# Performance work log

Measured on AMD Instinct MI355X. Metric: run time of the kernel, lower is better.

Reference implementation:

```python
import jax, jax.numpy as jnp
import numpy as np

B, S, D, H, DFF, L, R, V = 2, 1024, 1024, 16, 4096, 2, 3, 32000
HD = D // H


def layer_norm(x, g, b, eps=1e-5):
    mu = jnp.mean(x, axis=-1, keepdims=True)
    var = jnp.var(x, axis=-1, keepdims=True)
    return (x - mu) / jnp.sqrt(var + eps) * g + b


def recursion_block(x, mask, Wqkv, bqkv, Wo, bo, W1, b1, W2, b2, ln1_g, ln1_b, ln2_g, ln2_b):
    # shared pre-LN transformer stack of L layers, applied once per recursion step
    Bc, Sc, _ = x.shape
    scale = 1.0 / np.sqrt(HD).astype(np.float32)
    for l in range(L):
        h = layer_norm(x, ln1_g[l], ln1_b[l])
        qkv = h @ Wqkv[l] + bqkv[l]
        q, k, v = jnp.split(qkv, 3, axis=-1)
        q = q.reshape(Bc, Sc, H, HD).transpose(0, 2, 1, 3)
        k = k.reshape(Bc, Sc, H, HD).transpose(0, 2, 1, 3)
        v = v.reshape(Bc, Sc, H, HD).transpose(0, 2, 1, 3)
        scores = jnp.einsum('bhqd,bhkd->bhqk', q, k) * scale + mask
        attn = jax.nn.softmax(scores, axis=-1)
        o = jnp.einsum('bhqk,bhkd->bhqd', attn, v).transpose(0, 2, 1, 3).reshape(Bc, Sc, D)
        x = x + o @ Wo[l] + bo[l]
        h2 = layer_norm(x, ln2_g[l], ln2_b[l])
        x = x + jax.nn.gelu(h2 @ W1[l] + b1[l]) @ W2[l] + b2[l]
    return x


def setup_inputs() -> dict:
    key = jax.random.key(0)
    ks = jax.random.split(key, 12)
    n = lambda k, shape: (jax.random.normal(k, shape, jnp.float32) * 0.02)
    return {
        'input_ids': jax.random.randint(ks[0], (B, S), 0, V),
        'token_embed': n(ks[1], (V, D)),
        'pos_embed': n(ks[2], (S, D)),
        'Wqkv': n(ks[3], (L, D, 3 * D)), 'bqkv': jnp.zeros((L, 3 * D), jnp.float32),
        'Wo': n(ks[4], (L, D, D)), 'bo': jnp.zeros((L, D), jnp.float32),
        'W1': n(ks[5], (L, D, DFF)), 'b1': jnp.zeros((L, DFF), jnp.float32),
        'W2': n(ks[6], (L, DFF, D)), 'b2': jnp.zeros((L, D), jnp.float32),
        'ln1_g': jnp.ones((L, D), jnp.float32), 'ln1_b': jnp.zeros((L, D), jnp.float32),
        'ln2_g': jnp.ones((L, D), jnp.float32), 'ln2_b': jnp.zeros((L, D), jnp.float32),
        'final_g': jnp.ones((D,), jnp.float32), 'final_b': jnp.zeros((D,), jnp.float32),
        'Wr': n(ks[7], (D, R)), 'br': jnp.zeros((R,), jnp.float32),
    }


def reference(input_ids, token_embed, pos_embed, Wqkv, bqkv, Wo, bo, W1, b1, W2, b2,
              ln1_g, ln1_b, ln2_g, ln2_b, final_g, final_b, Wr, br):
    h = token_embed[input_ids] + pos_embed[None, :, :]            # [B,S,D]
    mask = jnp.where(jnp.tril(jnp.ones((S, S), bool)), 0.0, -jnp.inf)[None, None]  # [1,1,S,S]
    # token-choice router on detached hidden states
    rlogits = jax.lax.stop_gradient(h) @ Wr + br                  # [B,S,R]
    probs = jax.nn.softmax(rlogits, axis=-1)
    depth_map = jnp.argmax(rlogits, axis=-1) + 1                  # depths in 1..R
    importance = probs.mean(axis=(0, 1))
    router_loss = R * jnp.sum(importance ** 2)                    # load-balance aux loss
    res = h
    for step in range(R):
        step_mask = depth_map >= step + 1                         # [B,S] bool
        upd = recursion_block(res, mask, Wqkv, bqkv, Wo, bo, W1, b1, W2, b2,
                              ln1_g, ln1_b, ln2_g, ln2_b)
        res = jnp.where(step_mask[..., None], upd, res)
    hf = layer_norm(res, final_g, final_b)
    logits = hf @ token_embed.T                                   # tied lm_head
    return logits, depth_map, router_loss
```

## Files before the change

kernel.cpp:

```cpp
#include <hip/hip_runtime.h>
#include <hip/hip_bf16.h>

#define DD 1024
#define SS 1024
#define BB 2
#define HH 16
#define DFFN 4096
#define LLAYERS 2
#define RSTEPS 3
#define VV 32000
#define NTOK (BB*SS)

typedef __attribute__((ext_vector_type(8))) short s16x8;
typedef __attribute__((ext_vector_type(8))) __bf16 bf16x8;
typedef __attribute__((ext_vector_type(4))) float f32x4;

__device__ __forceinline__ unsigned short f2bf(float f) {
  unsigned int u = __float_as_uint(f);
  u += 0x7FFFu + ((u >> 16) & 1u);
  return (unsigned short)(u >> 16);
}

__device__ __forceinline__ f32x4 mfma16(s16x8 a, s16x8 b, f32x4 c) {
  return __builtin_amdgcn_mfma_f32_16x16x32_bf16(
      __builtin_bit_cast(bf16x8, a), __builtin_bit_cast(bf16x8, b), c, 0, 0, 0);
}

__device__ __forceinline__ void gload16(const unsigned short* g, unsigned short* l) {
  __builtin_amdgcn_global_load_lds(
      (const __attribute__((address_space(1))) unsigned int*)(const void*)g,
      (__attribute__((address_space(3))) unsigned int*)(void*)l, 16, 0, 0);
}

#define BAR()  asm volatile("s_barrier" ::: "memory")
#define LGK0() do { asm volatile("s_waitcnt lgkmcnt(0)" ::: "memory"); \
                    __builtin_amdgcn_sched_barrier(0); } while (0)
#define VM4()  asm volatile("s_waitcnt vmcnt(4)" ::: "memory")
#define VM0()  asm volatile("s_waitcnt vmcnt(0)" ::: "memory")

__global__ __launch_bounds__(256) void wtrans_all_kernel(
    const float* __restrict__ Wqkv, const float* __restrict__ Wo,
    const float* __restrict__ W1, const float* __restrict__ W2,
    const float* __restrict__ te,
    unsigned short* __restrict__ WqkvT, unsigned short* __restrict__ WoT,
    unsigned short* __restrict__ W1T, unsigned short* __restrict__ W2T,
    unsigned short* __restrict__ teb) {
  const int bid = blockIdx.x;
  const int tid = threadIdx.x;
  if (bid >= 6144) {
    long i = ((long)(bid - 6144) * 256 + tid) * 8;
    float4 v0 = *(const float4*)(te + i);
    float4 v1 = *(const float4*)(te + i + 4);
    ushort4 a, b;
    a.x = f2bf(v0.x); a.y = f2bf(v0.y); a.z = f2bf(v0.z); a.w = f2bf(v0.w);
    b.x = f2bf(v1.x); b.y = f2bf(v1.y); b.z = f2bf(v1.z); b.w = f2bf(v1.w);
    *(ushort4*)(teb + i) = a;
    *(ushort4*)(teb + i + 4) = b;
    return;
  }
  const float* src; unsigned short* dst; int Kd, Nd, local;
  if (bid < 1536) {
    int l = (bid >= 768);
    local = bid - l * 768;
    src = Wqkv + (long)l * DD * 3 * DD; dst = WqkvT + (long)l * 3 * DD * DD;
    Kd = DD; Nd = 3 * DD;
  } else if (bid < 2048) {
    int l = (bid - 1536) >> 8; local = (bid - 1536) & 255;
    src = Wo + (long)l * DD * DD; dst = WoT + (long)l * DD * DD;
    Kd = DD; Nd = DD;
  } else if (bid < 4096) {
    int l = (bid - 2048) >> 10; local = (bid - 2048) & 1023;
    src = W1 + (long)l * DD * DFFN; dst = W1T + (long)l * DFFN * DD;
    Kd = DD; Nd = DFFN;
  } else {
    int l = (bid - 4096) >> 10; local = (bid - 4096) & 1023;
    src = W2 + (long)l * DFFN * DD; dst = W2T + (long)l * DD * DFFN;
    Kd = DFFN; Nd = DD;
  }
  const int tn = Nd >> 6;
  const int n0 = (local % tn) * 64, k0 = (local / tn) * 64;
  __shared__ unsigned short t[64][68];
#pragma unroll
  for (int c = 0; c < 4; ++c) {
    int p = tid + c * 256;
    int kr = p >> 4, nc = (p & 15) * 4;
    float4 v = *(const float4*)(src + (long)(k0 + kr) * Nd + n0 + nc);
    t[nc + 0][kr] = f2bf(v.x);
    t[nc + 1][kr] = f2bf(v.y);
    t[nc + 2][kr] = f2bf(v.z);
    t[nc + 3][kr] = f2bf(v.w);
  }
  __syncthreads();
#pragma unroll
  for (int c = 0; c < 4; ++c) {
    int p = tid + c * 256;
    int nr = p >> 4, kc = (p & 15) * 4;
    ushort4 o;
    o.x = t[nr][kc]; o.y = t[nr][kc + 1]; o.z = t[nr][kc + 2]; o.w = t[nr][kc + 3];
    *(ushort4*)(dst + (long)(n0 + nr) * Kd + k0 + kc) = o;
  }
}

__global__ __launch_bounds__(256) void embed_router_kernel(
    const int* __restrict__ ids, const float* __restrict__ te,
    const float* __restrict__ pe, const float* __restrict__ Wr,
    const float* __restrict__ br, float* __restrict__ res,
    float* __restrict__ probs, float* __restrict__ depth_ws,
    float* __restrict__ out_depth) {
  int row = blockIdx.x;
  int s = row & (SS - 1);
  int id = ids[row];
  int t = threadIdx.x;
  int d = t * 4;
  float4 a = *(const float4*)(te + (long)id * DD + d);
  float4 p = *(const float4*)(pe + (long)s * DD + d);
  float4 o; o.x = a.x + p.x; o.y = a.y + p.y; o.z = a.z + p.z; o.w = a.w + p.w;
  *(float4*)(res + (long)row * DD + d) = o;
  float a0 = 0.f, a1 = 0.f, a2 = 0.f;
  float hv[4] = {o.x, o.y, o.z, o.w};
#pragma unroll
  for (int j = 0; j < 4; ++j) {
    int dd = d + j;
    a0 += hv[j] * Wr[dd * 3 + 0];
    a1 += hv[j] * Wr[dd * 3 + 1];
    a2 += hv[j] * Wr[dd * 3 + 2];
  }
  for (int off = 32; off; off >>= 1) {
    a0 += __shfl_down(a0, off);
    a1 += __shfl_down(a1, off);
    a2 += __shfl_down(a2, off);
  }
  __shared__ float red[4][3];
  int wave = t >> 6;
  if ((t & 63) == 0) { red[wave][0] = a0; red[wave][1] = a1; red[wave][2] = a2; }
  __syncthreads();
  if (t == 0) {
    a0 = red[0][0] + red[1][0] + red[2][0] + red[3][0] + br[0];
    a1 = red[0][1] + red[1][1] + red[2][1] + red[3][1] + br[1];
    a2 = red[0][2] + red[1][2] + red[2][2] + red[3][2] + br[2];
    float m = fmaxf(a0, fmaxf(a1, a2));
    float e0 = expf(a0 - m), e1 = expf(a1 - m), e2 = expf(a2 - m);
    float inv = 1.f / (e0 + e1 + e2);
    probs[row * 3 + 0] = e0 * inv;
    probs[row * 3 + 1] = e1 * inv;
    probs[row * 3 + 2] = e2 * inv;
    int am = 0; float bv = a0;
    if (a1 > bv) { bv = a1; am = 1; }
    if (a2 > bv) { bv = a2; am = 2; }
    float dm = (float)(am + 1);
    depth_ws[row] = dm;
    out_depth[row] = dm;
  }
}

__global__ __launch_bounds__(256) void router_finalize_kernel(
    const float* __restrict__ probs, float* __restrict__ out_loss) {
  __shared__ float red[256][3];
  int t = threadIdx.x;
  float s0 = 0.f, s1 = 0.f, s2 = 0.f;
  for (int r = t; r < NTOK; r += 256) {
    s0 += probs[r * 3 + 0]; s1 += probs[r * 3 + 1]; s2 += probs[r * 3 + 2];
  }
  red[t][0] = s0; red[t][1] = s1; red[t][2] = s2;
  __syncthreads();
  for (int off = 128; off; off >>= 1) {
    if (t < off) {
      red[t][0] += red[t + off][0];
      red[t][1] += red[t + off][1];
      red[t][2] += red[t + off][2];
    }
    __syncthreads();
  }
  if (t == 0) {
    float i0 = red[0][0] / NTOK, i1 = red[0][1] / NTOK, i2 = red[0][2] / NTOK;
    out_loss[0] = (float)RSTEPS * (i0 * i0 + i1 * i1 + i2 * i2);
  }
}

__global__ __launch_bounds__(256) void ln_kernel(
    const float* __restrict__ x, const float* __restrict__ g,
    const float* __restrict__ b, unsigned short* __restrict__ y) {
  int row = blockIdx.x;
  int t = threadIdx.x;
  float4 v = *(const float4*)(x + (long)row * DD + t * 4);
  float s = v.x + v.y + v.z + v.w;
  float q = v.x * v.x + v.y * v.y + v.z * v.z + v.w * v.w;
  for (int off = 32; off; off >>= 1) {
    s += __shfl_down(s, off);
    q += __shfl_down(q, off);
  }
  __shared__ float rs[4], rq[4];
  int wave = t >> 6;
  if ((t & 63) == 0) { rs[wave] = s; rq[wave] = q; }
  __syncthreads();
  float S_ = rs[0] + rs[1] + rs[2] + rs[3];
  float Q_ = rq[0] + rq[1] + rq[2] + rq[3];
  float mu = S_ * (1.f / DD);
  float var = Q_ * (1.f / DD) - mu * mu;
  float rstd = rsqrtf(var + 1e-5f);
  int d = t * 4;
  float4 gg = *(const float4*)(g + d);
  float4 bb = *(const float4*)(b + d);
  ushort4 ov;
  ov.x = f2bf((v.x - mu) * rstd * gg.x + bb.x);
  ov.y = f2bf((v.y - mu) * rstd * gg.y + bb.y);
  ov.z = f2bf((v.z - mu) * rstd * gg.z + bb.z);
  ov.w = f2bf((v.w - mu) * rstd * gg.w + bb.w);
  *(ushort4*)(y + (long)row * DD + d) = ov;
}

__device__ __forceinline__ void stageA8(unsigned short* S, int buf, int qm,
    const unsigned short* A, int lda, long m0, int kt, int tid) {
  unsigned short* dst = S + buf * 32768 + qm * 8192;
#pragma unroll
  for (int c = 0; c < 2; ++c) {
    int idx = tid + c * 512;
    int L = (idx << 4) ^ (((idx >> 5) & 1) << 5);
    int band = L >> 13, row = (L >> 7) & 63, kel = (L & 127) >> 1;
    gload16(A + (m0 + band * 128 + qm * 64 + row) * (long)lda + kt * 64 + kel,
            dst + idx * 8);
  }
}

__device__ __forceinline__ void stageB8(unsigned short* S, int buf, int qn,
    const unsigned short* Bt, int ldb, long n0, int kt, int tid) {
  unsigned short* dst = S + buf * 32768 + 16384 + qn * 8192;
#pragma unroll
  for (int c = 0; c < 2; ++c) {
    int idx = tid + c * 512;
    int L = (idx << 4) ^ (((idx >> 5) & 1) << 5);
    int band = L >> 12, row = (L >> 7) & 31, kel = (L & 127) >> 1;
    gload16(Bt + (n0 + band * 64 + qn * 32 + row) * (long)ldb + kt * 64 + kel,
            dst + idx * 8);
  }
}

__device__ __forceinline__ void read_af8(const unsigned short* S, int base,
    int wm, int l16, int g, s16x8 af[2][4]) {
  const int swz = ((l16 >> 2) & 1) << 5;
#pragma unroll
  for (int kk = 0; kk < 2; ++kk)
#pragma unroll
    for (int mf = 0; mf < 4; ++mf) {
      int L = (wm * 8192 + (mf * 16 + l16) * 128 + (kk * 32 + g * 8) * 2) ^ swz;
      af[kk][mf] = *(const s16x8*)(S + base + (L >> 1));
    }
}

__device__ __forceinline__ void read_bf8(const unsigned short* S, int base,
    int wn, int l16, int g, s16x8 bf[2][2]) {
  const int swz = ((l16 >> 2) & 1) << 5;
#pragma unroll
  for (int kk = 0; kk < 2; ++kk)
#pragma unroll
    for (int nf = 0; nf < 2; ++nf) {
      int L = (wn * 4096 + (nf * 16 + l16) * 128 + (kk * 32 + g * 8) * 2) ^ swz;
      bf[kk][nf] = *(const s16x8*)(S + base + (L >> 1));
    }
}

template<int QM, int QN>
__device__ __forceinline__ void do_mfma8(f32x4 acc[8][4],
    const s16x8 af[2][4], const s16x8 bf[2][2]) {
  __builtin_amdgcn_s_setprio(1);
#pragma unroll
  for (int kk = 0; kk < 2; ++kk)
#pragma unroll
    for (int mf = 0; mf < 4; ++mf)
#pragma unroll
      for (int nf = 0; nf < 2; ++nf)
        acc[QM * 4 + mf][QN * 2 + nf] =
            mfma16(af[kk][mf], bf[kk][nf], acc[QM * 4 + mf][QN * 2 + nf]);
  __builtin_amdgcn_s_setprio(0);
}

template<int CBF16, int BIAS, int GELU_ACT>
__global__ __launch_bounds__(512, 1) void gemm256_kernel(
    const unsigned short* __restrict__ A, int lda,
    const unsigned short* __restrict__ Bt, int ldb,
    void* __restrict__ Cv, int ldc,
    const float* __restrict__ bias, int K, int Mblocks) {
  __shared__ unsigned short S[65536];
  const int tid = threadIdx.x;
  const int lane = tid & 63, wave = tid >> 6;
  const int g = lane >> 4, l16 = lane & 15;
  const int wm = wave >> 2, wn = wave & 3;
  const int nwg = gridDim.x * gridDim.y;
  const int orig = blockIdx.x + blockIdx.y * gridDim.x;
  const int q = nwg >> 3, r = nwg & 7;
  const int xcd = orig & 7, loc = orig >> 3;
  const int wgid = (xcd < r ? xcd * (q + 1) : r * (q + 1) + (xcd - r) * q) + loc;
  const long m0 = (long)(wgid % Mblocks) * 256;
  const long n0 = (long)(wgid / Mblocks) * 256;

  f32x4 acc[8][4] = {};
  s16x8 af[2][4], bf[2][2];
  const int NI = K >> 7;

  stageA8(S, 0, 0, A, lda, m0, 0, tid);
  stageA8(S, 0, 1, A, lda, m0, 0, tid);
  stageB8(S, 0, 0, Bt, ldb, n0, 0, tid);
  stageB8(S, 0, 1, Bt, ldb, n0, 0, tid);
  stageA8(S, 1, 0, A, lda, m0, 1, tid);
  stageB8(S, 1, 1, Bt, ldb, n0, 1, tid);
  VM4(); BAR();

  for (int i = 0; i < NI; ++i) {
    const int kt1 = 2 * i + 1, kt2 = 2 * i + 2, kt3 = 2 * i + 3;
    const bool more = (i + 1 < NI);
    read_af8(S, 0, wm, l16, g, af);
    read_bf8(S, 16384, wn, l16, g, bf);
    stageA8(S, 1, 1, A, lda, m0, kt1, tid);
    BAR(); LGK0();
    do_mfma8<0, 0>(acc, af, bf);
    BAR();
    read_bf8(S, 16384 + 8192, wn, l16, g, bf);
    stageB8(S, 1, 0, Bt, ldb, n0, kt1, tid);
    BAR(); LGK0();
    do_mfma8<0, 1>(acc, af, bf);
    BAR();
    read_af8(S, 8192, wm, l16, g, af);
    if (more) stageA8(S, 0, 0, A, lda, m0, kt2, tid);
    BAR(); LGK0();
    do_mfma8<1, 1>(acc, af, bf);
    BAR();
    read_bf8(S, 16384, wn, l16, g, bf);
    if (more) stageB8(S, 0, 1, Bt, ldb, n0, kt2, tid);
    BAR(); LGK0();
    do_mfma8<1, 0>(acc, af, bf);
    if (more) { VM4(); } else { VM0(); }
    BAR();
    read_af8(S, 32768, wm, l16, g, af);
    read_bf8(S, 32768 + 16384, wn, l16, g, bf);
    if (more) stageA8(S, 0, 1, A, lda, m0, kt2, tid);
    BAR(); LGK0();
    do_mfma8<0, 0>(acc, af, bf);
    BAR();
    read_bf8(S, 32768 + 16384 + 8192, wn, l16, g, bf);
    if (more) stageB8(S, 0, 0, Bt, ldb, n0, kt2, tid);
    BAR(); LGK0();
    do_mfma8<0, 1>(acc, af, bf);
    BAR();
    read_af8(S, 32768 + 8192, wm, l16, g, af);
    if (more) stageA8(S, 1, 0, A, lda, m0, kt3, tid);
    BAR(); LGK0();
    do_mfma8<1, 1>(acc, af, bf);
    BAR();
    read_bf8(S, 32768 + 16384, wn, l16, g, bf);
    if (more) stageB8(S, 1, 1, Bt, ldb, n0, kt3, tid);
    BAR(); LGK0();
    do_mfma8<1, 0>(acc, af, bf);
    VM4(); BAR();
  }

#pragma unroll
  for (int mf = 0; mf < 8; ++mf) {
#pragma unroll
    for (int nf = 0; nf < 4; ++nf) {
      long row0 = m0 + wm * 128 + mf * 16 + g * 4;
      long col = n0 + wn * 64 + nf * 16 + l16;
      float bv = BIAS ? bias[col] : 0.f;
#pragma unroll
      for (int rr = 0; rr < 4; ++rr) {
        float v = acc[mf][nf][rr] + bv;
        if (GELU_ACT) {
          float x3 = v * v * v;
          v = 0.5f * v * (1.f + tanhf(0.7978845608028654f * (v + 0.044715f * x3)));
        }
        if (CBF16) ((unsigned short*)Cv)[(row0 + rr) * (long)ldc + col] = f2bf(v);
        else       ((float*)Cv)[(row0 + rr) * (long)ldc + col] = v;
      }
    }
  }
}

template<int BN, int CBF16, int BIAS, int RESID, int GELU_ACT, int SELW, int QKVW>
__global__ __launch_bounds__(256) void gemm128_kernel(
    const unsigned short* __restrict__ A, int lda,
    const unsigned short* __restrict__ Bt, int ldb,
    void* __restrict__ Cv, int ldc,
    const float* __restrict__ bias,
    const float* __restrict__ resid, int ldr,
    const float* __restrict__ depth_ws, float stepf,
    unsigned short* __restrict__ vtw,
    int K) {
  constexpr int BM = 128;
  constexpr int WN = BN / 2;
  constexpr int MR = 4;
  constexpr int NR = WN / 16;
  __shared__ unsigned short As[BM * 64];
  __shared__ unsigned short Bs[BN * 64];
  const int tid = threadIdx.x;
  const int lane = tid & 63, wave = tid >> 6;
  const int g = lane >> 4, l16 = lane & 15;
  const int wr = wave >> 1, wc = wave & 1;
  int lin = blockIdx.x + blockIdx.y * gridDim.x;
  int per = (gridDim.x * gridDim.y) >> 3;
  int v = (lin & 7) * per + (lin >> 3);
  const long m0 = (long)(v % gridDim.y) * BM;
  const long n0 = (long)(v / gridDim.y) * BN;
  f32x4 acc[MR][NR] = {};
  for (int k0 = 0; k0 < K; k0 += 64) {
    __syncthreads();
#pragma unroll
    for (int c = 0; c < BM / 32; ++c) {
      int p = tid + c * 256;
      int r = p >> 3, kq = (p & 7) * 8;
      gload16(A + (m0 + r) * (long)lda + k0 + kq, &As[p * 8]);
    }
#pragma unroll
    for (int c = 0; c < BN / 32; ++c) {
      int p = tid + c * 256;
      int r = p >> 3, kq = (p & 7) * 8;
      gload16(Bt + (n0 + r) * (long)ldb + k0 + kq, &Bs[p * 8]);
    }
    __syncthreads();
#pragma unroll
    for (int kk = 0; kk < 2; ++kk) {
      s16x8 af[MR], bf[NR];
#pragma unroll
      for (int m = 0; m < MR; ++m)
        af[m] = *(const s16x8*)&As[(wr * 64 + m * 16 + l16) * 64 + kk * 32 + g * 8];
#pragma unroll
      for (int n = 0; n < NR; ++n)
        bf[n] = *(const s16x8*)&Bs[(wc * WN + n * 16 + l16) * 64 + kk * 32 + g * 8];
#pragma unroll
      for (int m = 0; m < MR; ++m)
#pragma unroll
        for (int n = 0; n < NR; ++n)
          acc[m][n] = mfma16(af[m], bf[n], acc[m][n]);
    }
  }
  const bool vblk = QKVW && (n0 >= 2048);
#pragma unroll
  for (int m = 0; m < MR; ++m) {
#pragma unroll
    for (int n = 0; n < NR; ++n) {
      long row_base = m0 + wr * 64 + m * 16 + g * 4;
      long col = n0 + wc * WN + n * 16 + l16;
      float bv = BIAS ? bias[col] : 0.f;
      float vv4[4];
#pragma unroll
      for (int r = 0; r < 4; ++r) {
        long row = row_base + r;
        float vv = acc[m][n][r] + bv;
        if (RESID) vv += resid[row * (long)ldr + col];
        if (GELU_ACT) {
          float x3 = vv * vv * vv;
          vv = 0.5f * vv * (1.f + tanhf(0.7978845608028654f * (vv + 0.044715f * x3)));
        }
        vv4[r] = vv;
      }
      if (QKVW && vblk) {
        int rel = (int)col - 2048;
        int h = rel >> 6, d = rel & 63;
        int b = (int)(row_base >> 10);
        int s = (int)(row_base & 1023);
        ushort4 o;
        o.x = f2bf(vv4[0]); o.y = f2bf(vv4[1]);
        o.z = f2bf(vv4[2]); o.w = f2bf(vv4[3]);
        *(ushort4*)(vtw + (((long)(b * 16 + h) * 64 + d) * SS + s)) = o;
      } else {
#pragma unroll
        for (int r = 0; r < 4; ++r) {
          long row = row_base + r;
          if (SELW) {
            if (depth_ws[row] >= stepf)
              ((float*)Cv)[row * (long)ldc + col] = vv4[r];
          } else if (CBF16) {
            ((unsigned short*)Cv)[row * (long)ldc + col] = f2bf(vv4[r]);
          } else {
            ((float*)Cv)[row * (long)ldc + col] = vv4[r];
          }
        }
      }
    }
  }
}

__global__ __launch_bounds__(512) void attn_kernel(
    const unsigned short* __restrict__ qkv,
    const unsigned short* __restrict__ vt,
    unsigned short* __restrict__ o) {
  __shared__ unsigned short Ks[2][64 * 64];
  __shared__ unsigned short Vs[2][64 * 64];
  __shared__ unsigned short Pl[8][16][72];
  const int qb = blockIdx.x;
  const int bh = blockIdx.y;
  const int b = bh >> 4, h = bh & 15;
  const int tid = threadIdx.x, wave = tid >> 6, lane = tid & 63;
  const int g = lane >> 4, l16 = lane & 15;
  const float NEG_INF = -__builtin_inff();
  const int q0 = qb * 128;
  const int qrw = q0 + wave * 16;
  const long rowbase = (long)b * SS;
  const unsigned short* kbase = qkv + rowbase * 3072 + 1024 + h * 64;
  const unsigned short* vbase = vt + (long)bh * 64 * SS;

  const unsigned short* qptr = qkv + (rowbase + qrw + l16) * 3072 + h * 64;
  s16x8 qf0 = *(const s16x8*)(qptr + g * 8);
  s16x8 qf1 = *(const s16x8*)(qptr + 32 + g * 8);

  f32x4 oacc[4] = {};
  float mrun = NEG_INF, lrun = 0.f;

  const int ntile = q0 / 64 + 2;

  {
    int r = tid >> 3;
    int bo = (tid & 7) * 16;
    int sw = (bo ^ ((r & 7) << 4)) >> 1;
    gload16(kbase + (long)r * 3072 + sw, &Ks[0][tid * 8]);
    gload16(vbase + (long)r * SS + 0 + sw, &Vs[0][tid * 8]);
  }
  asm volatile("s_waitcnt vmcnt(0)" ::: "memory");
  __syncthreads();

  for (int t = 0; t < ntile; ++t) {
    const int cur = t & 1;
    const int kv0 = t * 64;
    const unsigned short* ks_cur = &Ks[cur][0];
    const unsigned short* vs_cur = &Vs[cur][0];
    if (t + 1 < ntile) {
      const int kvn = kv0 + 64;
      int r = tid >> 3;
      int bo = (tid & 7) * 16;
      int sw = (bo ^ ((r & 7) << 4)) >> 1;
      gload16(kbase + (long)(kvn + r) * 3072 + sw, &Ks[cur ^ 1][tid * 8]);
      gload16(vbase + (long)r * SS + kvn + sw, &Vs[cur ^ 1][tid * 8]);
    }
    f32x4 accs[4] = {};
#pragma unroll
    for (int ks = 0; ks < 2; ++ks) {
#pragma unroll
      for (int kvb = 0; kvb < 4; ++kvb) {
        int row = kvb * 16 + l16;
        int bo = ((ks * 64 + g * 16) ^ ((l16 & 7) << 4)) >> 1;
        s16x8 kf = *(const s16x8*)&ks_cur[row * 64 + bo];
        accs[kvb] = mfma16(kf, ks ? qf1 : qf0, accs[kvb]);
      }
    }
    const bool needmask = (kv0 + 63 > qrw);
    const int qabs = qrw + l16;
    float sv[4][4];
    float mloc = NEG_INF;
#pragma unroll
    for (int kvb = 0; kvb < 4; ++kvb) {
#pragma unroll
      for (int r = 0; r < 4; ++r) {
        float vv = accs[kvb][r] * 0.125f;
        if (needmask) {
          int kva = kv0 + kvb * 16 + g * 4 + r;
          if (kva > qabs) vv = NEG_INF;
        }
        sv[kvb][r] = vv;
        mloc = fmaxf(mloc, vv);
      }
    }
    mloc = fmaxf(mloc, __shfl_xor(mloc, 16));
    mloc = fmaxf(mloc, __shfl_xor(mloc, 32));
    float mnew = fmaxf(mrun, mloc);
    float alpha = __expf(mrun - mnew);
    float lsum = 0.f;
#pragma unroll
    for (int kvb = 0; kvb < 4; ++kvb) {
      float p0 = __expf(sv[kvb][0] - mnew);
      float p1 = __expf(sv[kvb][1] - mnew);
      float p2 = __expf(sv[kvb][2] - mnew);
      float p3 = __expf(sv[kvb][3] - mnew);
      lsum += (p0 + p1) + (p2 + p3);
      unsigned int w0 = (unsigned)f2bf(p0) | ((unsigned)f2bf(p1) << 16);
      unsigned int w1 = (unsigned)f2bf(p2) | ((unsigned)f2bf(p3) << 16);
      uint2 pw; pw.x = w0; pw.y = w1;
      *(uint2*)&Pl[wave][l16][kvb * 16 + g * 4] = pw;
    }
    lsum += __shfl_xor(lsum, 16);
    lsum += __shfl_xor(lsum, 32);
    lrun = lrun * alpha + lsum;
    mrun = mnew;
    float mult[4];
#pragma unroll
    for (int r = 0; r < 4; ++r) mult[r] = __shfl(alpha, g * 4 + r);
#pragma unroll
    for (int nd = 0; nd < 4; ++nd)
#pragma unroll
      for (int r = 0; r < 4; ++r) oacc[nd][r] *= mult[r];
#pragma unroll
    for (int kh = 0; kh < 2; ++kh) {
      s16x8 pa = *(const s16x8*)&Pl[wave][l16][kh * 32 + g * 8];
#pragma unroll
      for (int nd = 0; nd < 4; ++nd) {
        int row = nd * 16 + l16;
        int bo = ((kh * 64 + g * 16) ^ ((l16 & 7) << 4)) >> 1;
        s16x8 vf = *(const s16x8*)&vs_cur[row * 64 + bo];
        oacc[nd] = mfma16(pa, vf, oacc[nd]);
      }
    }
    asm volatile("s_waitcnt vmcnt(0)" ::: "memory");
    __syncthreads();
  }
  unsigned short* ob = o + (rowbase + qrw) * 1024 + h * 64;
#pragma unroll
  for (int r = 0; r < 4; ++r) {
    float lr = __shfl(lrun, g * 4 + r);
    float inv = 1.f / lr;
#pragma unroll
    for (int nd = 0; nd < 4; ++nd)
      ob[(long)(g * 4 + r) * 1024 + nd * 16 + l16] = f2bf(oacc[nd][r] * inv);
  }
}

extern "C" void kernel_launch(void* const* d_in, const int* in_sizes, int n_in,
                              void* d_out, int out_size, void* d_ws, size_t ws_size,
                              hipStream_t stream) {
  (void)in_sizes; (void)n_in; (void)out_size; (void)ws_size;
  const int*   ids  = (const int*)d_in[0];
  const float* te   = (const float*)d_in[1];
  const float* pe   = (const float*)d_in[2];
  const float* Wqkv = (const float*)d_in[3];
  const float* bqkv = (const float*)d_in[4];
  const float* Wo   = (const float*)d_in[5];
  const float* bo   = (const float*)d_in[6];
  const float* W1   = (const float*)d_in[7];
  const float* b1   = (const float*)d_in[8];
  const float* W2   = (const float*)d_in[9];
  const float* b2   = (const float*)d_in[10];
  const float* ln1g = (const float*)d_in[11];
  const float* ln1b = (const float*)d_in[12];
  const float* ln2g = (const float*)d_in[13];
  const float* ln2b = (const float*)d_in[14];
  const float* fing = (const float*)d_in[15];
  const float* finb = (const float*)d_in[16];
  const float* Wr   = (const float*)d_in[17];
  const float* br   = (const float*)d_in[18];

  float* logits    = (float*)d_out;
  float* out_depth = logits + (long)NTOK * VV;
  float* out_loss  = out_depth + NTOK;

  char* w = (char*)d_ws;
  float* res            = (float*)w;          w += (long)NTOK * DD * 4;
  float* x              = (float*)w;          w += (long)NTOK * DD * 4;
  unsigned short* hbuf  = (unsigned short*)w; w += (long)NTOK * DD * 2;
  unsigned short* qkvb  = (unsigned short*)w; w += (long)NTOK * 3 * DD * 2;
  unsigned short* obuf  = (unsigned short*)w; w += (long)NTOK * DD * 2;
  unsigned short* ffn1  = (unsigned short*)w; w += (long)NTOK * DFFN * 2;
  unsigned short* vtb   = (unsigned short*)w; w += (long)BB * HH * 64 * SS * 2;
  float* probs          = (float*)w;          w += (long)NTOK * 3 * 4;
  float* depth_ws       = (float*)w;          w += (long)NTOK * 4;
  unsigned short* WqkvT = (unsigned short*)w; w += (long)LLAYERS * 3 * DD * DD * 2;
  unsigned short* WoT   = (unsigned short*)w; w += (long)LLAYERS * DD * DD * 2;
  unsigned short* W1T   = (unsigned short*)w; w += (long)LLAYERS * DFFN * DD * 2;
  unsigned short* W2T   = (unsigned short*)w; w += (long)LLAYERS * DD * DFFN * 2;
  unsigned short* teb   = (unsigned short*)w; w += (long)VV * DD * 2;

  wtrans_all_kernel<<<6144 + 16000, 256, 0, stream>>>(
      Wqkv, Wo, W1, W2, te, WqkvT, WoT, W1T, W2T, teb);

  embed_router_kernel<<<NTOK, 256, 0, stream>>>(ids, te, pe, Wr, br,
                                                res, probs, depth_ws, out_depth);
  router_finalize_kernel<<<1, 256, 0, stream>>>(probs, out_loss);

  for (int step = 0; step < RSTEPS; ++step) {
    for (int l = 0; l < LLAYERS; ++l) {
      const float* xin = (l == 0) ? res : x;
      ln_kernel<<<NTOK, 256, 0, stream>>>(xin, ln1g + l * DD, ln1b + l * DD, hbuf);
      gemm128_kernel<128, 1, 1, 0, 0, 0, 1><<<dim3(3 * DD / 128, NTOK / 128), 256, 0, stream>>>(
          hbuf, DD, WqkvT + (long)l * 3 * DD * DD, DD, qkvb, 3 * DD,
          bqkv + (long)l * 3 * DD, nullptr, 0, nullptr, 0.f, vtb, DD);
      attn_kernel<<<dim3(SS / 128, BB * HH), 512, 0, stream>>>(qkvb, vtb, obuf);
      gemm128_kernel<64, 0, 1, 1, 0, 0, 0><<<dim3(DD / 64, NTOK / 128), 256, 0, stream>>>(
          obuf, DD, WoT + (long)l * DD * DD, DD, x, DD,
          bo + (long)l * DD, xin, DD, nullptr, 0.f, nullptr, DD);
      ln_kernel<<<NTOK, 256, 0, stream>>>(x, ln2g + l * DD, ln2b + l * DD, hbuf);
      gemm128_kernel<128, 1, 1, 0, 1, 0, 0><<<dim3(DFFN / 128, NTOK / 128), 256, 0, stream>>>(
          hbuf, DD, W1T + (long)l * DFFN * DD, DD, ffn1, DFFN,
          b1 + (long)l * DFFN, nullptr, 0, nullptr, 0.f, nullptr, DD);
      if (l == 0) {
        gemm128_kernel<64, 0, 1, 1, 0, 0, 0><<<dim3(DD / 64, NTOK / 128), 256, 0, stream>>>(
            ffn1, DFFN, W2T + (long)l * DD * DFFN, DFFN, x, DD,
            b2 + (long)l * DD, x, DD, nullptr, 0.f, nullptr, DFFN);
      } else {
        gemm128_kernel<64, 0, 1, 1, 0, 1, 0><<<dim3(DD / 64, NTOK / 128), 256, 0, stream>>>(
            ffn1, DFFN, W2T + (long)l * DD * DFFN, DFFN, res, DD,
            b2 + (long)l * DD, x, DD, depth_ws, (float)(step + 1), nullptr, DFFN);
      }
    }
  }
  ln_kernel<<<NTOK, 256, 0, stream>>>(res, fing, finb, hbuf);
  gemm256_kernel<0, 0, 0><<<dim3(VV / 256, NTOK / 256), 512, 0, stream>>>(
      hbuf, DD, teb, DD, logits, VV, nullptr, DD, NTOK / 256);
}
```

Before: 1.437 ms.

## Multi-stage pipelined GEMM with swizzled LDS, merge prep kernels, reverse attention order

Replaces the single-buffered 128-row GEMM with a 512-thread variant that prefetches K tiles into 2 or 3 LDS buffers, with explicit vmcnt waits and an XOR swizzle on LDS addresses to reduce bank conflicts. Each wave now computes a 32-row strip instead of 64. The embedding/router kernel is merged into the weight-conversion kernel to save a launch. The attention grid is reversed so the heaviest causal query blocks are scheduled first. The larger LDS footprint and 512-thread blocks may lower occupancy, and the hand-written wait counts must stay consistent with the per-thread load count.

```diff
diff --git a/kernel.cpp b/kernel.cpp
--- a/kernel.cpp
+++ b/kernel.cpp
@@ -38,15 +38,74 @@
 #define VM4()  asm volatile("s_waitcnt vmcnt(4)" ::: "memory")
 #define VM0()  asm volatile("s_waitcnt vmcnt(0)" ::: "memory")
 
-__global__ __launch_bounds__(256) void wtrans_all_kernel(
+template<int N> __device__ __forceinline__ void vmw() {
+  if constexpr (N == 0) asm volatile("s_waitcnt vmcnt(0)" ::: "memory");
+  else if constexpr (N == 3) asm volatile("s_waitcnt vmcnt(3)" ::: "memory");
+  else if constexpr (N == 4) asm volatile("s_waitcnt vmcnt(4)" ::: "memory");
+  else if constexpr (N == 6) asm volatile("s_waitcnt vmcnt(6)" ::: "memory");
+  else if constexpr (N == 8) asm volatile("s_waitcnt vmcnt(8)" ::: "memory");
+}
+
+__global__ __launch_bounds__(256) void prep_all_kernel(
     const float* __restrict__ Wqkv, const float* __restrict__ Wo,
     const float* __restrict__ W1, const float* __restrict__ W2,
     const float* __restrict__ te,
     unsigned short* __restrict__ WqkvT, unsigned short* __restrict__ WoT,
     unsigned short* __restrict__ W1T, unsigned short* __restrict__ W2T,
-    unsigned short* __restrict__ teb) {
+    unsigned short* __restrict__ teb,
+    const int* __restrict__ ids, const float* __restrict__ pe,
+    const float* __restrict__ Wr, const float* __restrict__ br,
+    float* __restrict__ res, float* __restrict__ probs,
+    float* __restrict__ depth_ws, float* __restrict__ out_depth) {
   const int bid = blockIdx.x;
   const int tid = threadIdx.x;
+  __shared__ unsigned short t[64][68];
+  __shared__ float red[4][3];
+  if (bid >= 22144) {
+    int row = bid - 22144;
+    int s = row & (SS - 1);
+    int id = ids[row];
+    int d = tid * 4;
+    float4 a = *(const float4*)(te + (long)id * DD + d);
+    float4 p = *(const float4*)(pe + (long)s * DD + d);
+    float4 o; o.x = a.x + p.x; o.y = a.y + p.y; o.z = a.z + p.z; o.w = a.w + p.w;
+    *(float4*)(res + (long)row * DD + d) = o;
+    float a0 = 0.f, a1 = 0.f, a2 = 0.f;
+    float hv[4] = {o.x, o.y, o.z, o.w};
+#pragma unroll
+    for (int j = 0; j < 4; ++j) {
+      int dd = d + j;
+      a0 += hv[j] * Wr[dd * 3 + 0];
+      a1 += hv[j] * Wr[dd * 3 + 1];
+      a2 += hv[j] * Wr[dd * 3 + 2];
+    }
+    for (int off = 32; off; off >>= 1) {
+      a0 += __shfl_down(a0, off);
+      a1 += __shfl_down(a1, off);
+      a2 += __shfl_down(a2, off);
+    }
+    int wave = tid >> 6;
+    if ((tid & 63) == 0) { red[wave][0] = a0; red[wave][1] = a1; red[wave][2] = a2; }
+    __syncthreads();
+    if (tid == 0) {
+      a0 = red[0][0] + red[1][0] + red[2][0] + red[3][0] + br[0];
+      a1 = red[0][1] + red[1][1] + red[2][1] + red[3][1] + br[1];
+      a2 = red[0][2] + red[1][2] + red[2][2] + red[3][2] + br[2];
+      float m = fmaxf(a0, fmaxf(a1, a2));
+      float e0 = expf(a0 - m), e1 = expf(a1 - m), e2 = expf(a2 - m);
+      float inv = 1.f / (e0 + e1 + e2);
+      probs[row * 3 + 0] = e0 * inv;
+      probs[row * 3 + 1] = e1 * inv;
+      probs[row * 3 + 2] = e2 * inv;
+      int am = 0; float bv = a0;
+      if (a1 > bv) { bv = a1; am = 1; }
+      if (a2 > bv) { bv = a2; am = 2; }
+      float dm = (float)(am + 1);
+      depth_ws[row] = dm;
+      out_depth[row] = dm;
+    }
+    return;
+  }
   if (bid >= 6144) {
     long i = ((long)(bid - 6144) * 256 + tid) * 8;
     float4 v0 = *(const float4*)(te + i);
@@ -79,7 +138,6 @@
   }
   const int tn = Nd >> 6;
   const int n0 = (local % tn) * 64, k0 = (local / tn) * 64;
-  __shared__ unsigned short t[64][68];
 #pragma unroll
   for (int c = 0; c < 4; ++c) {
     int p = tid + c * 256;
@@ -98,58 +156,6 @@
     ushort4 o;
     o.x = t[nr][kc]; o.y = t[nr][kc + 1]; o.z = t[nr][kc + 2]; o.w = t[nr][kc + 3];
     *(ushort4*)(dst + (long)(n0 + nr) * Kd + k0 + kc) = o;
-  }
-}
-
-__global__ __launch_bounds__(256) void embed_router_kernel(
-    const int* __restrict__ ids, const float* __restrict__ te,
-    const float* __restrict__ pe, const float* __restrict__ Wr,
-    const float* __restrict__ br, float* __restrict__ res,
-    float* __restrict__ probs, float* __restrict__ depth_ws,
-    float* __restrict__ out_depth) {
-  int row = blockIdx.x;
-  int s = row & (SS - 1);
-  int id = ids[row];
-  int t = threadIdx.x;
-  int d = t * 4;
-  float4 a = *(const float4*)(te + (long)id * DD + d);
-  float4 p = *(const float4*)(pe + (long)s * DD + d);
-  float4 o; o.x = a.x + p.x; o.y = a.y + p.y; o.z = a.z + p.z; o.w = a.w + p.w;
-  *(float4*)(res + (long)row * DD + d) = o;
-  float a0 = 0.f, a1 = 0.f, a2 = 0.f;
-  float hv[4] = {o.x, o.y, o.z, o.w};
-#pragma unroll
-  for (int j = 0; j < 4; ++j) {
-    int dd = d + j;
-    a0 += hv[j] * Wr[dd * 3 + 0];
-    a1 += hv[j] * Wr[dd * 3 + 1];
-    a2 += hv[j] * Wr[dd * 3 + 2];
-  }
-  for (int off = 32; off; off >>= 1) {
-    a0 += __shfl_down(a0, off);
-    a1 += __shfl_down(a1, off);
-    a2 += __shfl_down(a2, off);
-  }
-  __shared__ float red[4][3];
-  int wave = t >> 6;
-  if ((t & 63) == 0) { red[wave][0] = a0; red[wave][1] = a1; red[wave][2] = a2; }
-  __syncthreads();
-  if (t == 0) {
-    a0 = red[0][0] + red[1][0] + red[2][0] + red[3][0] + br[0];
-    a1 = red[0][1] + red[1][1] + red[2][1] + red[3][1] + br[1];
-    a2 = red[0][2] + red[1][2] + red[2][2] + red[3][2] + br[2];
-    float m = fmaxf(a0, fmaxf(a1, a2));
-    float e0 = expf(a0 - m), e1 = expf(a1 - m), e2 = expf(a2 - m);
-    float inv = 1.f / (e0 + e1 + e2);
-    probs[row * 3 + 0] = e0 * inv;
-    probs[row * 3 + 1] = e1 * inv;
-    probs[row * 3 + 2] = e2 * inv;
-    int am = 0; float bv = a0;
-    if (a1 > bv) { bv = a1; am = 1; }
-    if (a2 > bv) { bv = a2; am = 2; }
-    float dm = (float)(am + 1);
-    depth_ws[row] = dm;
-    out_depth[row] = dm;
   }
 }
 
@@ -374,8 +380,9 @@
   }
 }
 
-template<int BN, int CBF16, int BIAS, int RESID, int GELU_ACT, int SELW, int QKVW>
-__global__ __launch_bounds__(256) void gemm128_kernel(
+template<int BN, int DEPTH, int CBF16, int BIAS, int RESID, int GELU_ACT,
+         int SELW, int QKVW>
+__global__ __launch_bounds__(512) void gemm_db_kernel(
     const unsigned short* __restrict__ A, int lda,
     const unsigned short* __restrict__ Bt, int ldb,
     void* __restrict__ Cv, int ldc,
@@ -384,12 +391,13 @@
     const float* __restrict__ depth_ws, float stepf,
     unsigned short* __restrict__ vtw,
     int K) {
-  constexpr int BM = 128;
   constexpr int WN = BN / 2;
-  constexpr int MR = 4;
   constexpr int NR = WN / 16;
-  __shared__ unsigned short As[BM * 64];
-  __shared__ unsigned short Bs[BN * 64];
+  constexpr int ACH = 2;
+  constexpr int BCH = BN / 64;
+  constexpr int LPT = ACH + BCH;
+  __shared__ unsigned short As[DEPTH][128 * 64];
+  __shared__ unsigned short Bs[DEPTH][BN * 64];
   const int tid = threadIdx.x;
   const int lane = tid & 63, wave = tid >> 6;
   const int g = lane >> 4, l16 = lane & 15;
@@ -397,46 +405,75 @@
   int lin = blockIdx.x + blockIdx.y * gridDim.x;
   int per = (gridDim.x * gridDim.y) >> 3;
   int v = (lin & 7) * per + (lin >> 3);
-  const long m0 = (long)(v % gridDim.y) * BM;
+  const long m0 = (long)(v % gridDim.y) * 128;
   const long n0 = (long)(v / gridDim.y) * BN;
-  f32x4 acc[MR][NR] = {};
-  for (int k0 = 0; k0 < K; k0 += 64) {
-    __syncthreads();
-#pragma unroll
-    for (int c = 0; c < BM / 32; ++c) {
-      int p = tid + c * 256;
-      int r = p >> 3, kq = (p & 7) * 8;
-      gload16(A + (m0 + r) * (long)lda + k0 + kq, &As[p * 8]);
-    }
-#pragma unroll
-    for (int c = 0; c < BN / 32; ++c) {
-      int p = tid + c * 256;
-      int r = p >> 3, kq = (p & 7) * 8;
-      gload16(Bt + (n0 + r) * (long)ldb + k0 + kq, &Bs[p * 8]);
-    }
-    __syncthreads();
+  f32x4 acc[2][NR] = {};
+  const int NT = K >> 6;
+
+  auto stage = [&](int buf, int kt) {
+    const int k0 = kt * 64;
+#pragma unroll
+    for (int c = 0; c < ACH; ++c) {
+      int p = tid + c * 512;
+      int L = (p << 4) ^ (((p >> 5) & 1) << 5);
+      int row = L >> 7, kel = (L & 127) >> 1;
+      gload16(A + (m0 + row) * (long)lda + k0 + kel, &As[buf][p * 8]);
+    }
+#pragma unroll
+    for (int c = 0; c < BCH; ++c) {
+      int p = tid + c * 512;
+      int L = (p << 4) ^ (((p >> 5) & 1) << 5);
+      int row = L >> 7, kel = (L & 127) >> 1;
+      gload16(Bt + (n0 + row) * (long)ldb + k0 + kel, &Bs[buf][p * 8]);
+    }
+  };
+
+#pragma unroll
+  for (int j = 0; j < DEPTH - 1; ++j) stage(j, j);
+
+  int cur = 0;
+  const int swz = ((l16 >> 2) & 1) << 5;
+  for (int kt = 0; kt < NT; ++kt) {
+    const int rem = NT - 1 - kt;
+    if (rem >= DEPTH - 1) {
+      int tgt = cur + DEPTH - 1; if (tgt >= DEPTH) tgt -= DEPTH;
+      stage(tgt, kt + DEPTH - 1);
+      vmw<(DEPTH - 1) * LPT>();
+    } else if (DEPTH == 3 && rem == 1) {
+      vmw<LPT>();
+    } else {
+      vmw<0>();
+    }
+    BAR();
 #pragma unroll
     for (int kk = 0; kk < 2; ++kk) {
-      s16x8 af[MR], bf[NR];
-#pragma unroll
-      for (int m = 0; m < MR; ++m)
-        af[m] = *(const s16x8*)&As[(wr * 64 + m * 16 + l16) * 64 + kk * 32 + g * 8];
-#pragma unroll
-      for (int n = 0; n < NR; ++n)
-        bf[n] = *(const s16x8*)&Bs[(wc * WN + n * 16 + l16) * 64 + kk * 32 + g * 8];
-#pragma unroll
-      for (int m = 0; m < MR; ++m)
+      s16x8 af[2], bf[NR];
+#pragma unroll
+      for (int m = 0; m < 2; ++m) {
+        int L = (((wr * 32 + m * 16 + l16) << 7) + ((kk * 32 + g * 8) << 1)) ^ swz;
+        af[m] = *(const s16x8*)&As[cur][L >> 1];
+      }
+#pragma unroll
+      for (int n = 0; n < NR; ++n) {
+        int L = (((wc * WN + n * 16 + l16) << 7) + ((kk * 32 + g * 8) << 1)) ^ swz;
+        bf[n] = *(const s16x8*)&Bs[cur][L >> 1];
+      }
+#pragma unroll
+      for (int m = 0; m < 2; ++m)
 #pragma unroll
         for (int n = 0; n < NR; ++n)
           acc[m][n] = mfma16(af[m], bf[n], acc[m][n]);
     }
-  }
+    BAR();
+    ++cur; if (cur == DEPTH) cur = 0;
+  }
+
   const bool vblk = QKVW && (n0 >= 2048);
 #pragma unroll
-  for (int m = 0; m < MR; ++m) {
+  for (int m = 0; m < 2; ++m) {
 #pragma unroll
     for (int n = 0; n < NR; ++n) {
-      long row_base = m0 + wr * 64 + m * 16 + g * 4;
+      long row_base = m0 + wr * 32 + m * 16 + g * 4;
       long col = n0 + wc * WN + n * 16 + l16;
       float bv = BIAS ? bias[col] : 0.f;
       float vv4[4];
@@ -485,7 +522,7 @@
   __shared__ unsigned short Ks[2][64 * 64];
   __shared__ unsigned short Vs[2][64 * 64];
   __shared__ unsigned short Pl[8][16][72];
-  const int qb = blockIdx.x;
+  const int qb = gridDim.x - 1 - blockIdx.x;
   const int bh = blockIdx.y;
   const int b = bh >> 4, h = bh & 15;
   const int tid = threadIdx.x, wave = tid >> 6, lane = tid & 63;
@@ -654,34 +691,37 @@
   unsigned short* W2T   = (unsigned short*)w; w += (long)LLAYERS * DD * DFFN * 2;
   unsigned short* teb   = (unsigned short*)w; w += (long)VV * DD * 2;
 
-  wtrans_all_kernel<<<6144 + 16000, 256, 0, stream>>>(
-      Wqkv, Wo, W1, W2, te, WqkvT, WoT, W1T, W2T, teb);
-
-  embed_router_kernel<<<NTOK, 256, 0, stream>>>(ids, te, pe, Wr, br,
-                                                res, probs, depth_ws, out_depth);
+  prep_all_kernel<<<6144 + 16000 + NTOK, 256, 0, stream>>>(
+      Wqkv, Wo, W1, W2, te, WqkvT, WoT, W1T, W2T, teb,
+      ids, pe, Wr, br, res, probs, depth_ws, out_depth);
   router_finalize_kernel<<<1, 256, 0, stream>>>(probs, out_loss);
 
   for (int step = 0; step < RSTEPS; ++step) {
     for (int l = 0; l < LLAYERS; ++l) {
       const float* xin = (l == 0) ? res : x;
       ln_kernel<<<NTOK, 256, 0, stream>>>(xin, ln1g + l * DD, ln1b + l * DD, hbuf);
-      gemm128_kernel<128, 1, 1, 0, 0, 0, 1><<<dim3(3 * DD / 128, NTOK / 128), 256, 0, stream>>>(
+      gemm_db_kernel<128, 2, 1, 1, 0, 0, 0, 1>
+          <<<dim3(3 * DD / 128, NTOK / 128), 512, 0, stream>>>(
           hbuf, DD, WqkvT + (long)l * 3 * DD * DD, DD, qkvb, 3 * DD,
           bqkv + (long)l * 3 * DD, nullptr, 0, nullptr, 0.f, vtb, DD);
       attn_kernel<<<dim3(SS / 128, BB * HH), 512, 0, stream>>>(qkvb, vtb, obuf);
-      gemm128_kernel<64, 0, 1, 1, 0, 0, 0><<<dim3(DD / 64, NTOK / 128), 256, 0, stream>>>(
+      gemm_db_kernel<64, 3, 0, 1, 1, 0, 0, 0>
+          <<<dim3(DD / 64, NTOK / 128), 512, 0, stream>>>(
           obuf, DD, WoT + (long)l * DD * DD, DD, x, DD,
           bo + (long)l * DD, xin, DD, nullptr, 0.f, nullptr, DD);
       ln_kernel<<<NTOK, 256, 0, stream>>>(x, ln2g + l * DD, ln2b + l * DD, hbuf);
-      gemm128_kernel<128, 1, 1, 0, 1, 0, 0><<<dim3(DFFN / 128, NTOK / 128), 256, 0, stream>>>(
+      gemm_db_kernel<128, 2, 1, 1, 0, 1, 0, 0>
+          <<<dim3(DFFN / 128, NTOK / 128), 512, 0, stream>>>(
           hbuf, DD, W1T + (long)l * DFFN * DD, DD, ffn1, DFFN,
           b1 + (long)l * DFFN, nullptr, 0, nullptr, 0.f, nullptr, DD);
       if (l == 0) {
-        gemm128_kernel<64, 0, 1, 1, 0, 0, 0><<<dim3(DD / 64, NTOK / 128), 256, 0, stream>>>(
+        gemm_db_kernel<64, 3, 0, 1, 1, 0, 0, 0>
+            <<<dim3(DD / 64, NTOK / 128), 512, 0, stream>>>(
             ffn1, DFFN, W2T + (long)l * DD * DFFN, DFFN, x, DD,
             b2 + (long)l * DD, x, DD, nullptr, 0.f, nullptr, DFFN);
       } else {
-        gemm128_kernel<64, 0, 1, 1, 0, 1, 0><<<dim3(DD / 64, NTOK / 128), 256, 0, stream>>>(
+        gemm_db_kernel<64, 3, 0, 1, 1, 0, 1, 0>
+            <<<dim3(DD / 64, NTOK / 128), 512, 0, stream>>>(
             ffn1, DFFN, W2T + (long)l * DD * DFFN, DFFN, res, DD,
             b2 + (long)l * DD, x, DD, depth_ws, (float)(step + 1), nullptr, DFFN);
       }
```

After: 1.217 ms, median of 2. 1.18x faster.
